# Performance work log

Hardware: AMD Instinct MI355X
Metric: run time of the kernel (lower is better)

Reference implementation:

```python
import jax, jax.numpy as jnp
import numpy as np

B = 512      # batch
F = 512      # n_features
G = 32       # grid_size
N = G * G    # num_nodes = 1024
D = 64       # embed_dim
H = 64       # hidden_dim
C = 100      # n_classes
A = 8        # num_atoms in symbiotic basis
EPS = 1e-8
DEG_EPS = 1e-6


def _grid_mask():
    """4-neighborhood mask for a GxG grid, [N, N] float32."""
    m = np.zeros((N, N), dtype=np.float32)
    for i in range(N):
        r, c = divmod(i, G)
        if r > 0:
            m[i, i - G] = 1.0
        if r < G - 1:
            m[i, i + G] = 1.0
        if c > 0:
            m[i, i - 1] = 1.0
        if c < G - 1:
            m[i, i + 1] = 1.0
    return jnp.asarray(m)


def setup_inputs() -> dict:
    key = jax.random.key(0)
    ks = jax.random.split(key, 16)
    s = 0.05  # small init scale (stands in for kaiming init)
    return {
        "x": jax.random.normal(ks[0], (B, F), jnp.float32),
        "W_embed": jax.random.normal(ks[1], (F, N * D), jnp.float32) * s,
        "b_embed": jnp.zeros((N * D,), jnp.float32),
        "adj_weights": jax.random.normal(ks[2], (N, N), jnp.float32) * 0.1,
        "adj_mask": _grid_mask(),
        "W1": jax.random.normal(ks[3], (D, H), jnp.float32) * s,
        "b1": jnp.zeros((H,), jnp.float32),
        "W2": jax.random.normal(ks[4], (H, D), jnp.float32) * s,
        "b2": jnp.zeros((D,), jnp.float32),
        "basis": jax.random.normal(ks[5], (A, D), jnp.float32) * 0.5,
        "Wq": jax.random.normal(ks[6], (D, D), jnp.float32) * s,
        "Wk": jax.random.normal(ks[7], (D, D), jnp.float32) * s,
        "Wr1": jax.random.normal(ks[8], (N * D, 2 * H), jnp.float32) * s,
        "br1": jnp.zeros((2 * H,), jnp.float32),
        "Wr2": jax.random.normal(ks[9], (2 * H, C), jnp.float32) * s,
        "br2": jnp.zeros((C,), jnp.float32),
    }


def _gelu(v):
    return jax.nn.gelu(v, approximate=False)  # torch nn.GELU default (erf)


def reference(x, W_embed, b_embed, adj_weights, adj_mask, W1, b1, W2, b2,
              basis, Wq, Wk, Wr1, br1, Wr2, br2):
    plasticity = 1.0
    bsz = x.shape[0]
    # input embed -> [B, N, D]
    x_embed = (x @ W_embed + b_embed).reshape(bsz, N, D)
    # dynamic topology: sigmoid-gated, mask-multiplied, degree-normalized adjacency
    adj = jax.nn.sigmoid(adj_weights * plasticity) * adj_mask          # [N, N]
    deg = jnp.clip(adj.sum(axis=1, keepdims=True), DEG_EPS, None)
    adj = adj / deg
    # graph diffusion (shared adjacency across batch)
    x_agg = jnp.einsum('ij,bjd->bid', adj, x_embed)                    # [B, N, D]
    # node processor MLP
    x_proc = _gelu(x_agg @ W1 + b1) @ W2 + b2                          # [B, N, D]
    # symbiotic basis refinement on flattened rows [B*N, D]
    flat = x_proc.reshape(-1, D)
    Q = flat @ Wq                                                      # [B*N, D]
    K = basis @ Wk                                                     # [A, D]
    attn = (Q @ K.T) / (jnp.sqrt(jnp.float32(D)) + EPS)                # [B*N, A]
    weights = jax.nn.softmax(attn, axis=-1)
    x_clean = jnp.clip(weights @ basis, -5.0, 5.0)                     # [B*N, D]
    w_safe = weights + EPS
    entropy = -(w_safe * jnp.log(w_safe)).sum(-1).mean()
    gram = basis @ basis.T
    ortho = jnp.clip(jnp.sum((gram - jnp.eye(A, dtype=gram.dtype)) ** 2), 0.0, 10.0)
    # readout (dropout is identity in eval)
    x_flat = x_clean.reshape(bsz, N * D)
    logits = _gelu(x_flat @ Wr1 + br1) @ Wr2 + br2                     # [B, C]
    return (logits, entropy, ortho)
```

## Files before the change

kernel.cpp:

```cpp
#include <hip/hip_runtime.h>
#include <hip/hip_bf16.h>
#include <math.h>

#define Bb 512
#define Ff 512
#define Gg 32
#define Nn 1024
#define Dd 64
#define Hh 64
#define Cc 100
#define Aa 8
#define NDd 65536

typedef float  f32x4  __attribute__((ext_vector_type(4)));
typedef __bf16 bf16x8 __attribute__((ext_vector_type(8)));

static __device__ __forceinline__ unsigned short f2bf(float f) {
    __bf16 h = (__bf16)f;
    return __builtin_bit_cast(unsigned short, h);
}
static __device__ __forceinline__ float bf2f(unsigned short s) {
    unsigned u = ((unsigned)s) << 16;
    return __builtin_bit_cast(float, u);
}
static __device__ __forceinline__ float gelu_f(float v) {
    return 0.5f * v * (1.0f + erff(v * 0.7071067811865476f));
}
static __device__ __forceinline__ float gelu_fast(float v) {
    float z = 1.5957691216057308f * v * (1.0f + 0.044715f * v * v);
    return v / (1.0f + __expf(-z));
}
static __device__ __forceinline__ float sigm(float v) {
    return 1.0f / (1.0f + expf(-v));
}

__global__ void k_adj(const float* __restrict__ aw, float* __restrict__ adjw) {
    int i = blockIdx.x * 256 + threadIdx.x;
    if (i >= Nn) return;
    int r = i >> 5, c = i & 31;
    float s0 = 0.f, s1 = 0.f, s2 = 0.f, s3 = 0.f;
    if (r > 0)       s0 = sigm(aw[(size_t)i * Nn + i - Gg]);
    if (r < Gg - 1)  s1 = sigm(aw[(size_t)i * Nn + i + Gg]);
    if (c > 0)       s2 = sigm(aw[(size_t)i * Nn + i - 1]);
    if (c < Gg - 1)  s3 = sigm(aw[(size_t)i * Nn + i + 1]);
    float deg = fmaxf(s0 + s1 + s2 + s3, 1e-6f);
    float inv = 1.0f / deg;
    adjw[i * 4 + 0] = s0 * inv;
    adjw[i * 4 + 1] = s1 * inv;
    adjw[i * 4 + 2] = s2 * inv;
    adjw[i * 4 + 3] = s3 * inv;
}

__global__ void __launch_bounds__(512) k_prep(
        const float* __restrict__ W1, const float* __restrict__ b2,
        const float* __restrict__ W2, const float* __restrict__ Wq,
        const float* __restrict__ Wk, const float* __restrict__ basis,
        unsigned short* __restrict__ Kbf, float* __restrict__ bq,
        unsigned short* __restrict__ W1f, unsigned short* __restrict__ Wcf,
        float* __restrict__ ortho_out) {
    __shared__ float sb[Aa * Dd];
    __shared__ float sWc[Hh * Dd];
    __shared__ float sKb[Aa * Dd];
    int t = threadIdx.x;
    sb[t] = basis[t];
    __syncthreads();
    {
        int a = t >> 6, d = t & 63;
        float acc = 0.f;
        #pragma unroll 8
        for (int e = 0; e < Dd; ++e) acc += sb[a * 64 + e] * Wk[e * 64 + d];
        sKb[t] = acc;
    }
    for (int it = 0; it < 8; ++it) {
        int o = it * 512 + t;
        int i = o >> 6, j = o & 63;
        float acc = 0.f;
        #pragma unroll 8
        for (int e = 0; e < 64; ++e) acc += W2[i * 64 + e] * Wq[e * 64 + j];
        sWc[o] = acc;
    }
    if (t < 64) {
        float acc = 0.f;
        #pragma unroll 8
        for (int e = 0; e < 64; ++e) acc += b2[e] * Wq[e * 64 + t];
        bq[t] = acc;
    }
    __syncthreads();
    {
        int l = t & 63, ni = (t >> 6) & 3, kk = t >> 8;
        int col = ni * 16 + (l & 15);
        int kbase = kk * 32 + (l >> 4) * 8;
        #pragma unroll
        for (int j = 0; j < 8; ++j) {
            int k = kbase + j;
            W1f[t * 8 + j] = f2bf(W1[k * 64 + col]);
            Wcf[t * 8 + j] = f2bf(sWc[k * 64 + col]);
        }
    }
    if (t < 128) {
        int lane = t & 63;
        int a = lane & 15;
        int dbase = ((t >> 6) * 32) + (lane >> 4) * 8;
        unsigned short kp[8];
        #pragma unroll
        for (int j = 0; j < 8; ++j)
            kp[j] = (a < 8) ? f2bf(sKb[a * 64 + dbase + j] * 0.125f) : (unsigned short)0;
        *(int4*)(Kbf + (size_t)t * 8) = *(int4*)kp;
    }
    if (t < 64) {
        int i = t >> 3, j = t & 7;
        float gsum = 0.f;
        #pragma unroll 8
        for (int d = 0; d < 64; ++d) gsum += sb[i * 64 + d] * sb[j * 64 + d];
        float diff = gsum - (i == j ? 1.0f : 0.0f);
        float v = diff * diff;
        #pragma unroll
        for (int off = 32; off; off >>= 1) v += __shfl_down(v, off);
        if (t == 0) *ortho_out = fminf(fmaxf(v, 0.0f), 10.0f);
    }
}

__global__ void __launch_bounds__(256) k_prepBW(
        const float* __restrict__ basis, const float* __restrict__ Wr1,
        unsigned short* __restrict__ BWf) {
    __shared__ float sb[Aa * Dd];
    int t = threadIdx.x;
    sb[t] = basis[t];
    sb[t + 256] = basis[t + 256];
    __syncthreads();
    int kk = blockIdx.x >> 1, ch = blockIdx.x & 1;
    int lane = t & 63, nib = t >> 6;
    int l15 = lane & 15;
    int n = kk * 4 + (lane >> 4);
    int c = ch * 64 + nib * 16 + l15;
    float o[8] = {0, 0, 0, 0, 0, 0, 0, 0};
    for (int d = 0; d < 64; ++d) {
        float wv = Wr1[(size_t)(n * 64 + d) * 128 + c];
        #pragma unroll
        for (int j = 0; j < 8; ++j) o[j] += sb[j * 64 + d] * wv;
    }
    unsigned short p[8];
    #pragma unroll
    for (int j = 0; j < 8; ++j) p[j] = f2bf(o[j]);
    *(int4*)(BWf + ((size_t)(kk * 8 + ch * 4 + nib) * 64 + lane) * 8) = *(int4*)p;
}

__global__ void __launch_bounds__(256) k_xf(const float* __restrict__ x,
                                            unsigned short* __restrict__ xf) {
    int gid = blockIdx.x * 256 + threadIdx.x;
    int lane = gid & 63, slot = gid >> 6;
    int rt = slot >> 4, kk = slot & 15;
    int row = rt * 16 + (lane & 15), k0 = kk * 32 + (lane >> 4) * 8;
    const float* p = x + (size_t)row * Ff + k0;
    f32x4 v0 = *(const f32x4*)p;
    f32x4 v1 = *(const f32x4*)(p + 4);
    unsigned short o[8];
    o[0] = f2bf(v0.x); o[1] = f2bf(v0.y); o[2] = f2bf(v0.z); o[3] = f2bf(v0.w);
    o[4] = f2bf(v1.x); o[5] = f2bf(v1.y); o[6] = f2bf(v1.z); o[7] = f2bf(v1.w);
    *(int4*)(xf + (size_t)gid * 8) = *(int4*)o;
}

__global__ void __launch_bounds__(512) k_embed(
        const unsigned short* __restrict__ xf, const float* __restrict__ We,
        const float* __restrict__ be, unsigned short* __restrict__ xe) {
    __shared__ unsigned short blds_e[32768];
    int n0 = blockIdx.x * 64;
    int t = threadIdx.x;
    for (int it = 0; it < 16; ++it) {
        int e = it * 2048 + t * 4;
        int k = e >> 6, col = e & 63;
        f32x4 v = *(const f32x4*)(We + (size_t)k * NDd + n0 + col);
        unsigned short* p = blds_e + ((k >> 3) * 64 + col) * 8 + (k & 7);
        p[0] = f2bf(v.x); p[8] = f2bf(v.y); p[16] = f2bf(v.z); p[24] = f2bf(v.w);
    }
    __syncthreads();
    int lane = t & 63, w = t >> 6;
    int l15 = lane & 15, l4 = lane >> 4;
    for (int mt = 0; mt < 2; ++mt) {
        int rtb = mt * 16 + w * 2;
        f32x4 acc[2][4] = {};
        for (int kk = 0; kk < 16; ++kk) {
            bf16x8 a[2], b[4];
            a[0] = *(const bf16x8*)(xf + ((size_t)((rtb + 0) * 16 + kk) * 64 + lane) * 8);
            a[1] = *(const bf16x8*)(xf + ((size_t)((rtb + 1) * 16 + kk) * 64 + lane) * 8);
            int kg = kk * 4 + l4;
            #pragma unroll
            for (int ni = 0; ni < 4; ++ni)
                b[ni] = *(const bf16x8*)(blds_e + (kg * 64 + ni * 16 + l15) * 8);
            #pragma unroll
            for (int mi = 0; mi < 2; ++mi)
                #pragma unroll
                for (int ni = 0; ni < 4; ++ni)
                    acc[mi][ni] = __builtin_amdgcn_mfma_f32_16x16x32_bf16(
                        a[mi], b[ni], acc[mi][ni], 0, 0, 0);
        }
        #pragma unroll
        for (int ni = 0; ni < 4; ++ni) {
            float bias = be[n0 + ni * 16 + l15];
            #pragma unroll
            for (int mi = 0; mi < 2; ++mi) {
                int row0 = mt * 256 + w * 32 + mi * 16 + l4 * 4;
                #pragma unroll
                for (int r = 0; r < 4; ++r) {
                    float vv = acc[mi][ni][r] + bias;
                    xe[(size_t)(row0 + r) * NDd + n0 + ni * 16 + l15] = f2bf(vv);
                }
            }
        }
    }
}

__global__ void __launch_bounds__(256) k_fused2(
        const unsigned short* __restrict__ xe, const float* __restrict__ adjw,
        const unsigned short* __restrict__ W1f, const unsigned short* __restrict__ Wcf,
        const float* __restrict__ b1, const float* __restrict__ bq,
        const unsigned short* __restrict__ Kbf, unsigned short* __restrict__ w_out,
        float* __restrict__ ent_part) {
    __shared__ __align__(16) unsigned short sm2[16384];
    int t = threadIdx.x;
    int lane = t & 63, w = t >> 6;
    int l15 = lane & 15, g = lane >> 4;
    unsigned short* hbT = sm2 + w * 4096;
    unsigned short* qT  = hbT + 2048;

    int r0 = blockIdx.x * 128 + w * 32;
    const unsigned short* xb = xe + ((size_t)(r0 >> 10) << 16);
    int nbase = r0 & 1023;

    bf16x8 afrag[2][2];
    #pragma unroll
    for (int ni = 0; ni < 2; ++ni) {
        int n = nbase + ni * 16 + l15;
        f32x4 wv = *(const f32x4*)(adjw + n * 4);
        int nu = max(n - 32, 0), nd = min(n + 32, 1023);
        int nl = max(n - 1, 0),  nr = min(n + 1, 1023);
        #pragma unroll
        for (int kk = 0; kk < 2; ++kk) {
            int off = kk * 32 + g * 8;
            int4 eu = *(const int4*)(xb + nu * 64 + off);
            int4 ed = *(const int4*)(xb + nd * 64 + off);
            int4 el = *(const int4*)(xb + nl * 64 + off);
            int4 er = *(const int4*)(xb + nr * 64 + off);
            const unsigned short* su = (const unsigned short*)&eu;
            const unsigned short* sd = (const unsigned short*)&ed;
            const unsigned short* sl = (const unsigned short*)&el;
            const unsigned short* sr = (const unsigned short*)&er;
            bf16x8 af;
            #pragma unroll
            for (int j = 0; j < 8; ++j) {
                float v = wv.x * bf2f(su[j]) + wv.y * bf2f(sd[j])
                        + wv.z * bf2f(sl[j]) + wv.w * bf2f(sr[j]);
                af[j] = (__bf16)v;
            }
            afrag[ni][kk] = af;
        }
    }

    f32x4 acc1[4][2] = {};
    #pragma unroll
    for (int kk = 0; kk < 2; ++kk)
        #pragma unroll
        for (int mi = 0; mi < 4; ++mi) {
            bf16x8 aW = *(const bf16x8*)(W1f + ((kk * 4 + mi) * 64 + lane) * 8);
            #pragma unroll
            for (int ni = 0; ni < 2; ++ni)
                acc1[mi][ni] = __builtin_amdgcn_mfma_f32_16x16x32_bf16(
                    aW, afrag[ni][kk], acc1[mi][ni], 0, 0, 0);
        }

    #pragma unroll
    for (int mi = 0; mi < 4; ++mi) {
        f32x4 bv = *(const f32x4*)(b1 + mi * 16 + g * 4);
        int kk2 = mi >> 1;
        int gt  = ((mi & 1) << 1) + (g >> 1);
        int jb  = (g & 1) << 2;
        #pragma unroll
        for (int ni = 0; ni < 2; ++ni) {
            float h0 = gelu_fast(acc1[mi][ni][0] + bv[0]);
            float h1 = gelu_fast(acc1[mi][ni][1] + bv[1]);
            float h2 = gelu_fast(acc1[mi][ni][2] + bv[2]);
            float h3 = gelu_fast(acc1[mi][ni][3] + bv[3]);
            unsigned d0 = (unsigned)f2bf(h0) | ((unsigned)f2bf(h1) << 16);
            unsigned d1 = (unsigned)f2bf(h2) | ((unsigned)f2bf(h3) << 16);
            int base = ((kk2 * 2 + ni) * 64 + gt * 16 + l15) * 8 + jb;
            *(unsigned*)(hbT + base)     = d0;
            *(unsigned*)(hbT + base + 2) = d1;
        }
    }
    __builtin_amdgcn_sched_barrier(0);

    f32x4 acc2[4][2] = {};
    #pragma unroll
    for (int kk = 0; kk < 2; ++kk) {
        bf16x8 bf0 = *(const bf16x8*)(hbT + ((kk * 2 + 0) * 64 + lane) * 8);
        bf16x8 bf1 = *(const bf16x8*)(hbT + ((kk * 2 + 1) * 64 + lane) * 8);
        #pragma unroll
        for (int mi = 0; mi < 4; ++mi) {
            bf16x8 aW = *(const bf16x8*)(Wcf + ((kk * 4 + mi) * 64 + lane) * 8);
            acc2[mi][0] = __builtin_amdgcn_mfma_f32_16x16x32_bf16(aW, bf0, acc2[mi][0], 0, 0, 0);
            acc2[mi][1] = __builtin_amdgcn_mfma_f32_16x16x32_bf16(aW, bf1, acc2[mi][1], 0, 0, 0);
        }
    }
    #pragma unroll
    for (int mi = 0; mi < 4; ++mi) {
        f32x4 bv = *(const f32x4*)(bq + mi * 16 + g * 4);
        int kk2 = mi >> 1;
        int gt  = ((mi & 1) << 1) + (g >> 1);
        int jb  = (g & 1) << 2;
        #pragma unroll
        for (int ni = 0; ni < 2; ++ni) {
            float q0 = acc2[mi][ni][0] + bv[0];
            float q1 = acc2[mi][ni][1] + bv[1];
            float q2 = acc2[mi][ni][2] + bv[2];
            float q3 = acc2[mi][ni][3] + bv[3];
            unsigned d0 = (unsigned)f2bf(q0) | ((unsigned)f2bf(q1) << 16);
            unsigned d1 = (unsigned)f2bf(q2) | ((unsigned)f2bf(q3) << 16);
            int base = ((kk2 * 2 + ni) * 64 + gt * 16 + l15) * 8 + jb;
            *(unsigned*)(qT + base)     = d0;
            *(unsigned*)(qT + base + 2) = d1;
        }
    }
    __builtin_amdgcn_sched_barrier(0);

    f32x4 accA[2] = {};
    #pragma unroll
    for (int kk = 0; kk < 2; ++kk) {
        bf16x8 kf = *(const bf16x8*)(Kbf + (kk * 64 + lane) * 8);
        bf16x8 q0 = *(const bf16x8*)(qT + ((kk * 2 + 0) * 64 + lane) * 8);
        bf16x8 q1 = *(const bf16x8*)(qT + ((kk * 2 + 1) * 64 + lane) * 8);
        accA[0] = __builtin_amdgcn_mfma_f32_16x16x32_bf16(kf, q0, accA[0], 0, 0, 0);
        accA[1] = __builtin_amdgcn_mfma_f32_16x16x32_bf16(kf, q1, accA[1], 0, 0, 0);
    }

    float x0[4], x1[4];
    #pragma unroll
    for (int r = 0; r < 4; ++r) {
        x0[r] = __shfl_xor(accA[0][r], 16);
        x1[r] = __shfl_xor(accA[1][r], 16);
    }
    bool odd = (g & 1);
    float f[8];
    #pragma unroll
    for (int r = 0; r < 4; ++r) {
        f[r]     = odd ? x1[r] : accA[0][r];
        f[r + 4] = odd ? accA[1][r] : x0[r];
    }
    float mx = f[0];
    #pragma unroll
    for (int i = 1; i < 8; ++i) mx = fmaxf(mx, f[i]);
    float e[8], S = 0.f, T = 0.f;
    #pragma unroll
    for (int i = 0; i < 8; ++i) {
        e[i] = __expf(f[i] - mx);
        S += e[i];
        T += e[i] * (f[i] - mx);
    }
    float inv = 1.0f / S;
    float ent = __logf(S) - T * inv;
    unsigned short pk[8];
    #pragma unroll
    for (int i = 0; i < 8; ++i) pk[i] = f2bf(e[i] * inv);
    if (g < 2)
        *(int4*)(w_out + (size_t)(r0 + g * 16 + l15) * 8) = *(int4*)pk;
    float entc = (g < 2) ? ent : 0.0f;
    #pragma unroll
    for (int off = 32; off; off >>= 1) entc += __shfl_down(entc, off);
    if (lane == 0) ent_part[blockIdx.x * 4 + w] = entc;
}

__global__ void __launch_bounds__(256) k_rd(
        const unsigned short* __restrict__ w_flat,
        const unsigned short* __restrict__ BWf, float* __restrict__ Yp) {
    int mt = blockIdx.x & 3, kc = blockIdx.x >> 2;
    int t = threadIdx.x;
    int lane = t & 63, w = t >> 6;
    int l15 = lane & 15, l4 = lane >> 4;
    int rowbase = mt * 128 + w * 32;
    f32x4 acc[2][8] = {};
    for (int kkl = 0; kkl < 16; ++kkl) {
        int KK = kc * 16 + kkl;
        int kb = KK * 32 + l4 * 8;
        bf16x8 a[2];
        #pragma unroll
        for (int mi = 0; mi < 2; ++mi)
            a[mi] = *(const bf16x8*)(w_flat + (size_t)(rowbase + mi * 16 + l15) * 8192 + kb);
        #pragma unroll
        for (int ni = 0; ni < 8; ++ni) {
            bf16x8 bb = *(const bf16x8*)(BWf + ((size_t)(KK * 8 + ni) * 64 + lane) * 8);
            #pragma unroll
            for (int mi = 0; mi < 2; ++mi)
                acc[mi][ni] = __builtin_amdgcn_mfma_f32_16x16x32_bf16(
                    a[mi], bb, acc[mi][ni], 0, 0, 0);
        }
    }
    #pragma unroll
    for (int ni = 0; ni < 8; ++ni)
        #pragma unroll
        for (int mi = 0; mi < 2; ++mi)
            #pragma unroll
            for (int r = 0; r < 4; ++r) {
                int rr = rowbase + mi * 16 + l4 * 4 + r;
                Yp[(size_t)kc * 65536 + rr * 128 + ni * 16 + l15] = acc[mi][ni][r];
            }
}

__global__ void __launch_bounds__(128) k_fin(
        const float* __restrict__ Yp, const float* __restrict__ br1,
        const float* __restrict__ Wr2, const float* __restrict__ br2,
        const float* __restrict__ ent_part, float* __restrict__ out) {
    __shared__ float yL[128];
    __shared__ float eR[128];
    int m = blockIdx.x, t = threadIdx.x;
    float s = 0.f;
    #pragma unroll
    for (int kc = 0; kc < 16; ++kc) s += Yp[(size_t)kc * 65536 + m * 128 + t];
    yL[t] = gelu_f(s + br1[t]);
    if (m == 0) {
        float es = 0.f;
        for (int i = t; i < 16384; i += 128) es += ent_part[i];
        eR[t] = es;
    }
    __syncthreads();
    if (t < 100) {
        float acc = br2[t];
        #pragma unroll 8
        for (int k = 0; k < 128; ++k) acc += yL[k] * Wr2[k * 100 + t];
        out[m * 100 + t] = acc;
    }
    if (m == 0 && t == 0) {
        float tot = 0.f;
        #pragma unroll
        for (int i = 0; i < 128; ++i) tot += eR[i];
        out[51200] = tot * (1.0f / 524288.0f);
    }
}

extern "C" void kernel_launch(void* const* d_in, const int* in_sizes, int n_in,
                              void* d_out, int out_size, void* d_ws, size_t ws_size,
                              hipStream_t stream) {
    const float* x     = (const float*)d_in[0];
    const float* We    = (const float*)d_in[1];
    const float* be    = (const float*)d_in[2];
    const float* aw    = (const float*)d_in[3];
    const float* W1    = (const float*)d_in[5];
    const float* b1    = (const float*)d_in[6];
    const float* W2    = (const float*)d_in[7];
    const float* b2    = (const float*)d_in[8];
    const float* basis = (const float*)d_in[9];
    const float* Wq    = (const float*)d_in[10];
    const float* Wk    = (const float*)d_in[11];
    const float* Wr1   = (const float*)d_in[12];
    const float* br1   = (const float*)d_in[13];
    const float* Wr2   = (const float*)d_in[14];
    const float* br2   = (const float*)d_in[15];
    (void)in_sizes; (void)n_in;

    if (ws_size < (size_t)90000000) return;

    char* ws = (char*)d_ws;
    unsigned short* w_flat = (unsigned short*)(ws);
    unsigned short* BWf    = (unsigned short*)(ws + 8388608);
    float*          Yp     = (float*)(ws + 10485760);
    unsigned short* xe     = (unsigned short*)(ws + 16777216);
    char* smallp = ws + 16777216 + 67108864;
    float* adjw            = (float*)(smallp);
    unsigned short* Kbf    = (unsigned short*)(smallp + 16384);
    unsigned short* W1f    = (unsigned short*)(smallp + 18432);
    unsigned short* Wcf    = (unsigned short*)(smallp + 26624);
    float* bq              = (float*)(smallp + 34816);
    unsigned short* xf     = (unsigned short*)(smallp + 35072);
    float* ent_part        = (float*)(smallp + 35072 + 524288);

    float* out = (float*)d_out;
    float* ortho_slot = out + 51201;

    k_adj<<<4, 256, 0, stream>>>(aw, adjw);
    k_prep<<<1, 512, 0, stream>>>(W1, b2, W2, Wq, Wk, basis, Kbf, bq, W1f, Wcf, ortho_slot);
    k_prepBW<<<512, 256, 0, stream>>>(basis, Wr1, BWf);
    k_xf<<<128, 256, 0, stream>>>(x, xf);
    k_embed<<<1024, 512, 0, stream>>>(xf, We, be, xe);
    k_fused2<<<4096, 256, 0, stream>>>(xe, adjw, W1f, Wcf, b1, bq, Kbf, w_flat, ent_part);
    k_rd<<<64, 256, 0, stream>>>(w_flat, BWf, Yp);
    k_fin<<<512, 128, 0, stream>>>(Yp, br1, Wr2, br2, ent_part, out);
}
```

Baseline: 225.8 us.

## Halve embed column tile and remap prepBW to one block per node

k_embed now processes 32 output columns per block instead of 64. That halves shared memory, doubles the grid to 2048 blocks, and changes the W_embed staging so each thread gathers 8 consecutive k rows and packs them into one 128-bit LDS store. k_prepBW now launches one 128-thread block per node, with coalesced reads of Wr1 rows and a recomputed output index. The aim is more occupancy and cheaper LDS staging. In exchange, each A fragment from xf is reused across fewer N columns, so global traffic for xf doubles.

```diff
diff --git a/kernel.cpp b/kernel.cpp
--- a/kernel.cpp
+++ b/kernel.cpp
@@ -120,29 +120,28 @@
     }
 }
 
-__global__ void __launch_bounds__(256) k_prepBW(
+__global__ void __launch_bounds__(128) k_prepBW(
         const float* __restrict__ basis, const float* __restrict__ Wr1,
         unsigned short* __restrict__ BWf) {
     __shared__ float sb[Aa * Dd];
     int t = threadIdx.x;
-    sb[t] = basis[t];
-    sb[t + 256] = basis[t + 256];
+    sb[t] = basis[t];         sb[t + 128] = basis[t + 128];
+    sb[t + 256] = basis[t + 256]; sb[t + 384] = basis[t + 384];
     __syncthreads();
-    int kk = blockIdx.x >> 1, ch = blockIdx.x & 1;
-    int lane = t & 63, nib = t >> 6;
-    int l15 = lane & 15;
-    int n = kk * 4 + (lane >> 4);
-    int c = ch * 64 + nib * 16 + l15;
-    float o[8] = {0, 0, 0, 0, 0, 0, 0, 0};
+    int n = blockIdx.x;
+    float acc[8] = {0, 0, 0, 0, 0, 0, 0, 0};
+    const float* wr = Wr1 + (size_t)n * 64 * 128 + t;
     for (int d = 0; d < 64; ++d) {
-        float wv = Wr1[(size_t)(n * 64 + d) * 128 + c];
-        #pragma unroll
-        for (int j = 0; j < 8; ++j) o[j] += sb[j * 64 + d] * wv;
+        float v = wr[(size_t)d * 128];
+        #pragma unroll
+        for (int a = 0; a < 8; ++a) acc[a] += sb[a * 64 + d] * v;
     }
     unsigned short p[8];
     #pragma unroll
-    for (int j = 0; j < 8; ++j) p[j] = f2bf(o[j]);
-    *(int4*)(BWf + ((size_t)(kk * 8 + ch * 4 + nib) * 64 + lane) * 8) = *(int4*)p;
+    for (int a = 0; a < 8; ++a) p[a] = f2bf(acc[a]);
+    int ni = t >> 4, l15 = t & 15;
+    *(int4*)(BWf + ((size_t)(((n >> 2) * 8 + ni) * 64) + (n & 3) * 16 + l15) * 8)
+        = *(int4*)p;
 }
 
 __global__ void __launch_bounds__(256) k_xf(const float* __restrict__ x,
@@ -163,39 +162,45 @@
 __global__ void __launch_bounds__(512) k_embed(
         const unsigned short* __restrict__ xf, const float* __restrict__ We,
         const float* __restrict__ be, unsigned short* __restrict__ xe) {
-    __shared__ unsigned short blds_e[32768];
-    int n0 = blockIdx.x * 64;
+    __shared__ unsigned short blds_e[16384];
+    int n0 = blockIdx.x * 32;
     int t = threadIdx.x;
-    for (int it = 0; it < 16; ++it) {
-        int e = it * 2048 + t * 4;
-        int k = e >> 6, col = e & 63;
-        f32x4 v = *(const f32x4*)(We + (size_t)k * NDd + n0 + col);
-        unsigned short* p = blds_e + ((k >> 3) * 64 + col) * 8 + (k & 7);
-        p[0] = f2bf(v.x); p[8] = f2bf(v.y); p[16] = f2bf(v.z); p[24] = f2bf(v.w);
+    {
+        int colS = t & 31, koS = t >> 5;
+        #pragma unroll
+        for (int it = 0; it < 4; ++it) {
+            int oct = it * 16 + koS;
+            const float* src = We + (size_t)(oct * 8) * NDd + n0 + colS;
+            unsigned short pk[8];
+            #pragma unroll
+            for (int j = 0; j < 8; ++j)
+                pk[j] = f2bf(src[(size_t)j * NDd]);
+            *(int4*)(blds_e + ((oct * 32 + colS) << 3)) = *(int4*)pk;
+        }
     }
     __syncthreads();
     int lane = t & 63, w = t >> 6;
     int l15 = lane & 15, l4 = lane >> 4;
     for (int mt = 0; mt < 2; ++mt) {
         int rtb = mt * 16 + w * 2;
-        f32x4 acc[2][4] = {};
+        f32x4 acc[2][2] = {};
+        #pragma unroll 4
         for (int kk = 0; kk < 16; ++kk) {
-            bf16x8 a[2], b[4];
+            bf16x8 a[2], b[2];
             a[0] = *(const bf16x8*)(xf + ((size_t)((rtb + 0) * 16 + kk) * 64 + lane) * 8);
             a[1] = *(const bf16x8*)(xf + ((size_t)((rtb + 1) * 16 + kk) * 64 + lane) * 8);
             int kg = kk * 4 + l4;
-            #pragma unroll
-            for (int ni = 0; ni < 4; ++ni)
-                b[ni] = *(const bf16x8*)(blds_e + (kg * 64 + ni * 16 + l15) * 8);
+            b[0] = *(const bf16x8*)(blds_e + (kg * 32 + l15) * 8);
+            b[1] = *(const bf16x8*)(blds_e + (kg * 32 + 16 + l15) * 8);
             #pragma unroll
             for (int mi = 0; mi < 2; ++mi)
                 #pragma unroll
-                for (int ni = 0; ni < 4; ++ni)
+                for (int ni = 0; ni < 2; ++ni)
                     acc[mi][ni] = __builtin_amdgcn_mfma_f32_16x16x32_bf16(
                         a[mi], b[ni], acc[mi][ni], 0, 0, 0);
         }
         #pragma unroll
-        for (int ni = 0; ni < 4; ++ni) {
+        for (int ni = 0; ni < 2; ++ni) {
             float bias = be[n0 + ni * 16 + l15];
             #pragma unroll
             for (int mi = 0; mi < 2; ++mi) {
@@ -476,9 +481,9 @@
 
     k_adj<<<4, 256, 0, stream>>>(aw, adjw);
     k_prep<<<1, 512, 0, stream>>>(W1, b2, W2, Wq, Wk, basis, Kbf, bq, W1f, Wcf, ortho_slot);
-    k_prepBW<<<512, 256, 0, stream>>>(basis, Wr1, BWf);
+    k_prepBW<<<1024, 128, 0, stream>>>(basis, Wr1, BWf);
     k_xf<<<128, 256, 0, stream>>>(x, xf);
-    k_embed<<<1024, 512, 0, stream>>>(xf, We, be, xe);
+    k_embed<<<2048, 512, 0, stream>>>(xf, We, be, xe);
     k_fused2<<<4096, 256, 0, stream>>>(xe, adjw, W1f, Wcf, b1, bq, Kbf, w_flat, ent_part);
     k_rd<<<64, 256, 0, stream>>>(w_flat, BWf, Yp);
     k_fin<<<512, 128, 0, stream>>>(Yp, br1, Wr2, br2, ent_part, out);
```

After: 226.1 us. No clear change (+0.1%).
